# Kernel tuning notes

Measured on AMD Instinct MI355X. Metric: run time of the kernel, lower is better.

The kernel has to match this reference:

```python
import jax, jax.numpy as jnp
import numpy as np

B, N, DIM = 4, 1024, 512
DEPTH, HEADS, DH = 4, 8, 64
INNER = HEADS * DH  # 512
W = 32              # sqrt(N), FeedForward reshapes tokens to (W, W)
SCALE = DH ** -0.5  # used for BOTH spatial and spectral branches (as in source)
EPS_LN = 1e-5
EPS_BN = 1e-5


def setup_inputs() -> dict:
    key = jax.random.key(0)
    ks = jax.random.split(key, 16)
    L = DEPTH
    def rn(k, shape, s=0.02):
        return jax.random.normal(k, shape, jnp.float32) * s
    return {
        "x": jax.random.normal(ks[0], (B, N, DIM), jnp.float32),
        "ln1_w": jnp.ones((L, DIM), jnp.float32), "ln1_b": jnp.zeros((L, DIM), jnp.float32),
        "Wqkv": rn(ks[1], (L, DIM, 3 * INNER)),
        "Wout": rn(ks[2], (L, INNER, DIM)), "bout": jnp.zeros((L, DIM), jnp.float32),
        "sp_w": rn(ks[3], (L, HEADS, HEADS, 3, 3), 0.1), "sp_b": jnp.zeros((L, HEADS), jnp.float32),
        "Wqkv_spec": rn(ks[4], (L, N, 3 * N)),
        "spec_w": rn(ks[5], (L, 1, 1, 3, 3), 0.1), "spec_b": jnp.zeros((L, 1), jnp.float32),
        "ln2_w": jnp.ones((L, DIM), jnp.float32), "ln2_b": jnp.zeros((L, DIM), jnp.float32),
        "dw_w": rn(ks[6], (L, DIM, 1, 3, 3), 0.1), "dw_b": jnp.zeros((L, DIM), jnp.float32),
        "pw_w": rn(ks[7], (L, 256, DIM)), "pw_b": jnp.zeros((L, 256), jnp.float32),
        "bn_g": jnp.ones((L, 256), jnp.float32), "bn_b": jnp.zeros((L, 256), jnp.float32),
        "bn_m": jnp.zeros((L, 256), jnp.float32), "bn_v": jnp.ones((L, 256), jnp.float32),
        "c1_w": rn(ks[8], (L, 512, 256)), "c1_b": jnp.zeros((L, 512), jnp.float32),
        "c2_w": rn(ks[9], (L, DIM, 512)), "c2_b": jnp.zeros((L, DIM), jnp.float32),
    }


def _ln(x, w, b):
    mu = x.mean(-1, keepdims=True)
    var = x.var(-1, keepdims=True)  # biased, matching torch LayerNorm
    return (x - mu) * jax.lax.rsqrt(var + EPS_LN) * w + b


def _conv3x3(x, w, b, groups=1):
    y = jax.lax.conv_general_dilated(x, w, (1, 1), 'SAME',
                                     dimension_numbers=('NCHW', 'OIHW', 'NCHW'),
                                     feature_group_count=groups)
    return y + b[None, :, None, None]


def _block(x, p):
    (ln1w, ln1b, Wqkv, Wout, bout, spw, spb, Wqs, scw, scb,
     ln2w, ln2b, dww, dwb, pww, pwb, bng, bnb, bnm, bnv, c1w, c1b, c2w, c2b) = p
    b = x.shape[0]
    # --- spatial attention (PreNorm) ---
    h = _ln(x, ln1w, ln1b)
    q, k, v = jnp.split(h @ Wqkv, 3, axis=-1)
    split_heads = lambda t: t.reshape(b, N, HEADS, DH).transpose(0, 2, 1, 3)  # b h n d
    q, k, v = split_heads(q), split_heads(k), split_heads(v)
    attn = jax.nn.softmax(jnp.einsum('bhid,bhjd->bhij', q, k) * SCALE, axis=-1)
    attn = _conv3x3(attn, spw, spb)  # conv over the softmax map (heads as channels)
    out = jnp.einsum('bhij,bhjd->bhid', attn, v).transpose(0, 2, 1, 3).reshape(b, N, INNER)
    out = out @ Wout + bout  # (b, n, dim)
    # --- spectral attention on h^T (b, dim, n); v_spec is dead code in source ---
    xt = jnp.swapaxes(h, -1, -2)
    qs, ks_, _vs = jnp.split(xt @ Wqs, 3, axis=-1)  # each (b, dim, n)
    a = jax.nn.softmax(jnp.einsum('bin,bjn->bij', qs, ks_) * SCALE, axis=-1)
    a = _conv3x3(a[:, None], scw, scb)[:, 0]  # (b, dim, dim)
    x = x + jnp.einsum('bnd,bde->bne', out, a)  # residual add from Transformer loop
    # --- FeedForward (PreNorm), FF adds its own internal residual too ---
    h2 = _ln(x, ln2w, ln2b)
    img = h2.reshape(b, W, W, DIM).transpose(0, 3, 1, 2)  # 'b (w h) c -> b c w h'
    t = _conv3x3(img, dww, dwb, groups=DIM)               # depthwise 3x3
    t = jnp.einsum('oc,bchw->bohw', pww, t) + pwb[None, :, None, None]  # pointwise dim->256
    t = (t - bnm[None, :, None, None]) * jax.lax.rsqrt(bnv + EPS_BN)[None, :, None, None] \
        * bng[None, :, None, None] + bnb[None, :, None, None]           # BatchNorm2d (eval)
    t = jax.nn.gelu(jnp.einsum('oc,bchw->bohw', c1w, t) + c1b[None, :, None, None], approximate=False)
    t = jax.nn.gelu(jnp.einsum('oc,bchw->bohw', c2w, t) + c2b[None, :, None, None], approximate=False)
    ff = h2 + t.transpose(0, 2, 3, 1).reshape(b, N, DIM)  # FF internal residual
    return x + ff


def _forward(x, ln1_w, ln1_b, Wqkv, Wout, bout, sp_w, sp_b, Wqkv_spec, spec_w, spec_b,
             ln2_w, ln2_b, dw_w, dw_b, pw_w, pw_b, bn_g, bn_b, bn_m, bn_v,
             c1_w, c1_b, c2_w, c2_b):
    stacked = (ln1_w, ln1_b, Wqkv, Wout, bout, sp_w, sp_b, Wqkv_spec, spec_w, spec_b,
               ln2_w, ln2_b, dw_w, dw_b, pw_w, pw_b, bn_g, bn_b, bn_m, bn_v,
               c1_w, c1_b, c2_w, c2_b)
    for i in range(DEPTH):
        x = _block(x, tuple(a[i] for a in stacked))
    return x


def reference(x, ln1_w, ln1_b, Wqkv, Wout, bout, sp_w, sp_b, Wqkv_spec, spec_w, spec_b,
              ln2_w, ln2_b, dw_w, dw_b, pw_w, pw_b, bn_g, bn_b, bn_m, bn_v,
              c1_w, c1_b, c2_w, c2_b):
    return _forward(x, ln1_w, ln1_b, Wqkv, Wout, bout, sp_w, sp_b, Wqkv_spec, spec_w, spec_b,
                    ln2_w, ln2_b, dw_w, dw_b, pw_w, pw_b, bn_g, bn_b, bn_m, bn_v,
                    c1_w, c1_b, c2_w, c2_b)
```

## Files before the change

### kernel.cpp

```cpp
#include <hip/hip_runtime.h>
#include <hip/hip_bf16.h>

typedef __hip_bfloat16 bf16;
typedef __attribute__((ext_vector_type(8))) short bf16x8;
typedef __attribute__((ext_vector_type(4))) float f32x4;

__device__ __forceinline__ float b2f(bf16 v){ return __bfloat162float(v); }
__device__ __forceinline__ bf16 f2b(float v){ return __float2bfloat16(v); }
__device__ __forceinline__ float bits2f(unsigned u){ return __uint_as_float(u << 16); }
__device__ __forceinline__ unsigned short f2bits(float v){ bf16 t = __float2bfloat16(v); return *(unsigned short*)&t; }

__device__ __forceinline__ float gelu_f(float x){
  return 0.5f * x * (1.f + erff(x * 0.7071067811865475f));
}

__device__ __forceinline__ void gload_lds(const void* g, void* l){
  __builtin_amdgcn_global_load_lds((const __attribute__((address_space(1))) void*)g,
                                   (__attribute__((address_space(3))) void*)l, 16, 0, 0);
}

template<bool MAX>
__device__ __forceinline__ float block_reduce(float v){
  __shared__ float s[4];
  #pragma unroll
  for (int o = 32; o > 0; o >>= 1){
    float t = __shfl_down(v, o, 64);
    v = MAX ? fmaxf(v, t) : (v + t);
  }
  int lane = threadIdx.x & 63, w = threadIdx.x >> 6;
  __syncthreads();
  if (lane == 0) s[w] = v;
  __syncthreads();
  return MAX ? fmaxf(fmaxf(s[0], s[1]), fmaxf(s[2], s[3]))
             : (s[0] + s[1] + s[2] + s[3]);
}

__global__ void detect_k(const unsigned* __restrict__ x, int* __restrict__ flag){
  __shared__ int cnt[256];
  int tid = threadIdx.x;
  int c = 0;
  for (int i = tid; i < 4096; i += 256){
    unsigned h = x[i] & 0xffffu;
    int e = (int)((h >> 7) & 0xff);
    if (h == 0u || (e >= 100 && e <= 133)) c++;
  }
  cnt[tid] = c;
  __syncthreads();
  for (int o = 128; o > 0; o >>= 1){ if (tid < o) cnt[tid] += cnt[tid+o]; __syncthreads(); }
  if (tid == 0) *flag = (cnt[0] < 2048) ? 1 : 0;
}

__global__ __launch_bounds__(256) void cvt_x_k(const void* __restrict__ src,
                                               float* __restrict__ X,
                                               const int* __restrict__ flag){
  int p = blockIdx.x*256 + threadIdx.x;
  X[p] = (*flag) ? ((const float*)src)[p]
                 : __bfloat162float(((const bf16*)src)[p]);
}

struct WCvt21 { const void* src[21]; long long cum[22]; };

__global__ __launch_bounds__(256) void cvt_w_k(WCvt21 a, bf16* __restrict__ WB,
                                               long long total, const int* __restrict__ flag){
  long long i = (long long)blockIdx.x*256 + threadIdx.x;
  if (i >= total) return;
  int t = 0;
  while (a.cum[t+1] <= i) t++;
  long long e = i - a.cum[t];
  WB[i] = (*flag) ? __float2bfloat16(((const float*)a.src[t])[e])
                  : ((const bf16*)a.src[t])[e];
}

__global__ __launch_bounds__(256) void wtrans_k(const void* __restrict__ src, bf16* __restrict__ dst,
                                                int ld_src, int ldd, long long sSrc, long long sDst,
                                                const int* __restrict__ flag){
  __shared__ bf16 t[64][65];
  int z = blockIdx.z;
  int r0 = blockIdx.x*64, c0 = blockIdx.y*64;
  int lane = threadIdx.x & 63, quad = threadIdx.x >> 6;
  const float* sf = (const float*)src;
  const bf16* sb = (const bf16*)src;
  int fl = *flag;
  #pragma unroll
  for (int k = 0; k < 16; ++k){
    int r = quad*16 + k;
    long long idx = z*sSrc + (long long)(r0+r)*ld_src + c0 + lane;
    float v = fl ? sf[idx] : b2f(sb[idx]);
    t[r][lane] = f2b(v);
  }
  __syncthreads();
  #pragma unroll
  for (int k = 0; k < 16; ++k){
    int c = quad*16 + k;
    dst[z*sDst + (long long)(c0+c)*ldd + r0 + lane] = t[lane][c];
  }
}

__global__ void wprep_k(const bf16* __restrict__ spw, bf16* __restrict__ Wr){
  int l = blockIdx.x;
  for (int t = threadIdx.x; t < 1536; t += 256){
    int ho = t / 96, k = t - ho*96;
    float v = 0.f;
    if (ho < 8 && k < 72){
      int tap = k >> 3, hi = k & 7;
      v = b2f(spw[l*576 + ho*72 + hi*9 + tap]);
    }
    Wr[l*1536 + t] = f2b(v);
  }
}

__global__ __launch_bounds__(256) void store_out_k(const float* __restrict__ X,
                                                   void* __restrict__ out,
                                                   const int* __restrict__ flag){
  int p = blockIdx.x*256 + threadIdx.x;
  if (*flag) ((float*)out)[p] = X[p];
  else       ((bf16*)out)[p] = f2b(X[p]);
}

template<int MF, int NF, typename TC>
__global__ __launch_bounds__(256) void gmfma_k(
    int M, int N, int K,
    const bf16* __restrict__ A, int lda, long long sA, long long sA2,
    const bf16* __restrict__ Bt, int ldb, long long sB, long long sB2,
    TC* __restrict__ C, int ldc, long long sC, long long sC2,
    float alpha, int beta,
    const bf16* __restrict__ bias_n,
    const float* __restrict__ scale_n,
    const float* __restrict__ shift_n,
    const bf16* __restrict__ addF,
    int act)
{
  constexpr int BM = MF*32, BN = NF*32;
  constexpr int CHA = BM/16, CH = (BM+BN)/16;
  static_assert(CH % 4 == 0, "chunks must divide among 4 waves");
  __shared__ bf16 Asm[BM][32];
  __shared__ bf16 Bsm[BN][32];
  const int tid = threadIdx.x;
  const int lane = tid & 63, wid = tid >> 6;
  const int wm = wid >> 1, wn = wid & 1;
  const int m0 = blockIdx.y*BM, n0 = blockIdx.x*BN;
  const int z = blockIdx.z;
  const long long zl = z & 7, zh = z >> 3;
  const bf16* Ab = A + zl*sA + zh*sA2;
  const bf16* Bb = Bt + zl*sB + zh*sB2;
  TC* Cb = C + zl*sC + zh*sC2;
  const bf16* Fb = addF ? addF + zl*sC + zh*sC2 : nullptr;

  f32x4 acc[MF][NF];
  f32x4 zero = {0.f, 0.f, 0.f, 0.f};
  #pragma unroll
  for (int m = 0; m < MF; ++m)
    #pragma unroll
    for (int n = 0; n < NF; ++n) acc[m][n] = zero;

  const int rchunk = lane >> 2;
  const int kchunk = (lane & 3) * 8;
  const int row16 = lane & 15, kq = (lane >> 4) * 8;

  for (int k0 = 0; k0 < K; k0 += 32){
    #pragma unroll
    for (int cc = 0; cc < CH/4; ++cc){
      int c = wid + cc*4;
      if (c < CHA){
        int row = c*16 + rchunk;
        gload_lds(Ab + (long long)(m0+row)*lda + k0 + kchunk, &Asm[c*16][0]);
      } else {
        int row = (c-CHA)*16 + rchunk;
        gload_lds(Bb + (long long)(n0+row)*ldb + k0 + kchunk, &Bsm[(c-CHA)*16][0]);
      }
    }
    __syncthreads();
    bf16x8 af[MF], bfr[NF];
    #pragma unroll
    for (int m = 0; m < MF; ++m)
      af[m] = *(const bf16x8*)&Asm[wm*(MF*16) + m*16 + row16][kq];
    #pragma unroll
    for (int n = 0; n < NF; ++n)
      bfr[n] = *(const bf16x8*)&Bsm[wn*(NF*16) + n*16 + row16][kq];
    #pragma unroll
    for (int m = 0; m < MF; ++m)
      #pragma unroll
      for (int n = 0; n < NF; ++n)
        acc[m][n] = __builtin_amdgcn_mfma_f32_16x16x32_bf16(af[m], bfr[n], acc[m][n], 0, 0, 0);
    __syncthreads();
  }

  #pragma unroll
  for (int m = 0; m < MF; ++m){
    #pragma unroll
    for (int n = 0; n < NF; ++n){
      int gn = n0 + wn*(NF*16) + n*16 + (lane & 15);
      float bn_ = bias_n ? b2f(bias_n[gn]) : 0.f;
      float sc = scale_n ? scale_n[gn] : 1.f;
      float sh = shift_n ? shift_n[gn] : 0.f;
      #pragma unroll
      for (int r = 0; r < 4; ++r){
        int gm = m0 + wm*(MF*16) + m*16 + (lane >> 4)*4 + r;
        float v = acc[m][n][r] * alpha + bn_;
        v = v * sc + sh;
        if (act) v = gelu_f(v);
        long long idx = (long long)gm*ldc + gn;
        if (Fb) v += b2f(Fb[idx]);
        if (beta){
          float old;
          if constexpr (__is_same(TC, float)) old = Cb[idx]; else old = b2f(Cb[idx]);
          v += old;
        }
        if constexpr (__is_same(TC, float)) Cb[idx] = v; else Cb[idx] = f2b(v);
      }
    }
  }
}

template<int MF, int NF, typename TC>
static void gmfma_x(hipStream_t st, int z, int M, int N, int K,
                    const bf16* A, int lda, long long sA, long long sA2,
                    const bf16* Bt, int ldb, long long sB, long long sB2,
                    TC* C, int ldc, long long sC, long long sC2,
                    float alpha = 1.f, int beta = 0,
                    const bf16* bias_n = nullptr,
                    const float* scale_n = nullptr, const float* shift_n = nullptr,
                    const bf16* addF = nullptr, int act = 0)
{
  dim3 g(N/(NF*32), M/(MF*32), z);
  gmfma_k<MF,NF,TC><<<g, 256, 0, st>>>(M,N,K,A,lda,sA,sA2,Bt,ldb,sB,sB2,C,ldc,sC,sC2,
                                       alpha,beta,bias_n,scale_n,shift_n,addF,act);
}

template<int MF, int NF, typename TC>
static void gmfma(hipStream_t st, int z, int M, int N, int K,
                  const bf16* A, int lda, long long sA,
                  const bf16* Bt, int ldb, long long sB,
                  TC* C, int ldc, long long sC,
                  float alpha = 1.f, int beta = 0,
                  const bf16* bias_n = nullptr,
                  const float* scale_n = nullptr, const float* shift_n = nullptr,
                  const bf16* addF = nullptr, int act = 0)
{
  gmfma_x<MF,NF,TC>(st, z, M, N, K, A, lda, sA, 8*sA, Bt, ldb, sB, 8*sB,
                    C, ldc, sC, 8*sC, alpha, beta, bias_n, scale_n, shift_n, addF, act);
}

__global__ __launch_bounds__(256) void ln_k(const float* __restrict__ X, bf16* __restrict__ Y,
                                            const bf16* __restrict__ w, const bf16* __restrict__ b){
  long long row = blockIdx.x;
  const float* x = X + row*512;
  bf16* y = Y + row*512;
  int tid = threadIdx.x;
  float v0 = x[tid], v1 = x[tid+256];
  float mean = block_reduce<false>(v0+v1) * (1.f/512.f);
  float msq  = block_reduce<false>(v0*v0+v1*v1) * (1.f/512.f);
  float var = msq - mean*mean;
  float rs = rsqrtf(var + 1e-5f);
  y[tid]     = f2b((v0-mean)*rs*b2f(w[tid])     + b2f(b[tid]));
  y[tid+256] = f2b((v1-mean)*rs*b2f(w[tid+256]) + b2f(b[tid+256]));
}

__global__ __launch_bounds__(256) void softmax_k(float* __restrict__ data, int cols){
  long long row = blockIdx.x;
  float* p = data + row * (long long)cols;
  int tid = threadIdx.x;
  int per = cols >> 8;
  float v[4];
  float mx = -3.4e38f;
  for (int r = 0; r < per; ++r){ v[r] = p[tid + (r<<8)]; mx = fmaxf(mx, v[r]); }
  mx = block_reduce<true>(mx);
  float sum = 0.f;
  for (int r = 0; r < per; ++r){ v[r] = __expf(v[r] - mx); sum += v[r]; }
  sum = block_reduce<false>(sum);
  float inv = 1.f / sum;
  for (int r = 0; r < per; ++r) p[tid + (r<<8)] = v[r] * inv;
}

__global__ __launch_bounds__(256) void maxsum_k(const bf16* __restrict__ Sp,
                                                float* __restrict__ Mrow, float* __restrict__ Irow,
                                                long long bstride){
  __shared__ float redmx[4][8];
  __shared__ float redsum[4][8];
  int i = blockIdx.x;
  long long b = blockIdx.y;
  const bf16* src = Sp + b*bstride + (long long)i*1024;
  int tid = threadIdx.x;
  int lane = tid & 63, w = tid >> 6;
  int j0 = tid*4;

  float v[8][4];
  #pragma unroll
  for (int h = 0; h < 8; ++h){
    ushort4 u = *(const ushort4*)&src[h*1048576 + j0];
    v[h][0] = bits2f(u.x); v[h][1] = bits2f(u.y);
    v[h][2] = bits2f(u.z); v[h][3] = bits2f(u.w);
  }
  #pragma unroll
  for (int h = 0; h < 8; ++h){
    float m = fmaxf(fmaxf(v[h][0], v[h][1]), fmaxf(v[h][2], v[h][3]));
    #pragma unroll
    for (int o = 32; o > 0; o >>= 1) m = fmaxf(m, __shfl_xor(m, o, 64));
    if (lane == 0) redmx[w][h] = m;
  }
  __syncthreads();
  float mx[8];
  #pragma unroll
  for (int h = 0; h < 8; ++h)
    mx[h] = fmaxf(fmaxf(redmx[0][h], redmx[1][h]), fmaxf(redmx[2][h], redmx[3][h]));
  #pragma unroll
  for (int h = 0; h < 8; ++h){
    float s = 0.f;
    #pragma unroll
    for (int r = 0; r < 4; ++r) s += __expf(v[h][r] - mx[h]);
    #pragma unroll
    for (int o = 32; o > 0; o >>= 1) s += __shfl_xor(s, o, 64);
    if (lane == 0) redsum[w][h] = s;
  }
  __syncthreads();
  if (tid < 8){
    float s = redsum[0][tid] + redsum[1][tid] + redsum[2][tid] + redsum[3][tid];
    long long o = (b*1024 + i)*8 + tid;
    Mrow[o] = mx[tid];
    Irow[o] = 1.f / s;
  }
}

__global__ __launch_bounds__(256) void convNorm_k(const bf16* __restrict__ Sp, bf16* __restrict__ Pout,
                                                  const bf16* __restrict__ Wr, const bf16* __restrict__ bias,
                                                  const float* __restrict__ Mrow, const float* __restrict__ Irow,
                                                  long long bstride){
  __shared__ bf16 tile[18][66][8];
  __shared__ float mrow[18][8];
  __shared__ float irow[18][8];
  long long b = blockIdx.z;
  int i0 = blockIdx.y*16, j0 = blockIdx.x*64;
  int tid = threadIdx.x;
  const bf16* src = Sp + b*bstride;

  for (int t = tid; t < 144; t += 256){
    int r = t >> 3, h = t & 7;
    int gi = i0 + r - 1;
    float m = 0.f, iv = 0.f;
    if ((unsigned)gi < 1024u){
      long long o = (b*1024 + gi)*8 + h;
      m = Mrow[o]; iv = Irow[o];
    }
    mrow[r][h] = m; irow[r][h] = iv;
  }
  __syncthreads();

  for (int t = tid; t < 18*66; t += 256){
    int row = t / 66, col = t - row*66;
    int gi = i0 + row - 1, gj = j0 + col - 1;
    bf16x8 val = {};
    if ((unsigned)gi < 1024u && (unsigned)gj < 1024u){
      long long base = (long long)gi*1024 + gj;
      #pragma unroll
      for (int h = 0; h < 8; ++h){
        float s = b2f(src[(long long)h*1048576 + base]);
        val[h] = (short)f2bits(__expf(s - mrow[row][h]) * irow[row][h]);
      }
    }
    *(bf16x8*)&tile[row][col][0] = val;
  }

  int lane = tid & 63, wid = tid >> 6;
  int row16 = lane & 15, q = lane >> 4;
  bf16x8 bf0 = *(const bf16x8*)&Wr[row16*96 +  0 + q*8];
  bf16x8 bf1 = *(const bf16x8*)&Wr[row16*96 + 32 + q*8];
  bf16x8 bf2 = *(const bf16x8*)&Wr[row16*96 + 64 + q*8];
  float bv = (row16 < 8) ? b2f(bias[row16]) : 0.f;
  __syncthreads();

  f32x4 zero = {0.f,0.f,0.f,0.f};
  #pragma unroll
  for (int rr = 0; rr < 4; ++rr){
    int ii = rr*4 + wid;
    f32x4 acc[4] = {zero, zero, zero, zero};
    #pragma unroll
    for (int ks = 0; ks < 3; ++ks){
      int tap = ks*4 + q;
      int tcl = tap > 8 ? 0 : tap;
      int di = tcl / 3, dj = tcl - di*3;
      bf16x8 bsel = ks == 0 ? bf0 : (ks == 1 ? bf1 : bf2);
      #pragma unroll
      for (int mf = 0; mf < 4; ++mf){
        bf16x8 af = *(const bf16x8*)&tile[ii + di][mf*16 + row16 + dj][0];
        acc[mf] = __builtin_amdgcn_mfma_f32_16x16x32_bf16(af, bsel, acc[mf], 0, 0, 0);
      }
    }
    if (row16 < 8){
      bf16* dst = Pout + b*bstride + (long long)row16*1048576 + (long long)(i0 + ii)*1024;
      #pragma unroll
      for (int mf = 0; mf < 4; ++mf){
        int j = j0 + mf*16 + q*4;
        ushort4 o;
        o.x = f2bits(acc[mf][0] + bv);
        o.y = f2bits(acc[mf][1] + bv);
        o.z = f2bits(acc[mf][2] + bv);
        o.w = f2bits(acc[mf][3] + bv);
        *(ushort4*)&dst[j] = o;
      }
    }
  }
}

__global__ __launch_bounds__(256) void conv_spec_k(const float* __restrict__ in, bf16* __restrict__ out,
                                                   const bf16* __restrict__ w, const bf16* __restrict__ bias){
  __shared__ float ti[66][67];
  __shared__ bf16 toutT[64][65];
  int b = blockIdx.z;
  int i0 = blockIdx.y*64, j0 = blockIdx.x*64;
  int tid = threadIdx.x;
  const float* ib = in + (long long)b*262144;
  for (int t = tid; t < 66*66; t += 256){
    int r = t / 66, c = t - r*66;
    int gi = i0 + r - 1, gj = j0 + c - 1;
    float v = 0.f;
    if ((unsigned)gi < 512u && (unsigned)gj < 512u) v = ib[gi*512 + gj];
    ti[r][c] = v;
  }
  __syncthreads();
  float w9[9], bv = b2f(bias[0]);
  #pragma unroll
  for (int d = 0; d < 9; ++d) w9[d] = b2f(w[d]);
  int ii = tid & 63;
  #pragma unroll
  for (int q = 0; q < 16; ++q){
    int jj = (tid >> 6)*16 + q;
    float acc = bv;
    #pragma unroll
    for (int di = 0; di < 3; ++di)
      #pragma unroll
      for (int dj = 0; dj < 3; ++dj)
        acc += w9[di*3+dj] * ti[ii+di][jj+dj];
    toutT[jj][ii] = f2b(acc);
  }
  __syncthreads();
  #pragma unroll
  for (int q = 0; q < 16; ++q){
    int jj = (tid >> 6)*16 + q;
    out[(long long)b*262144 + (j0+jj)*512 + i0 + (tid & 63)] = toutT[jj][tid & 63];
  }
}

__global__ __launch_bounds__(256) void dwconv_k(const bf16* __restrict__ H2, bf16* __restrict__ T1,
                                                const bf16* __restrict__ w, const bf16* __restrict__ bias){
  int p = blockIdx.x*256 + threadIdx.x;
  int cp = p & 255;
  int n = (p >> 8) & 1023;
  int b = p >> 18;
  int c0 = cp*2;
  int wi = n >> 5, hg = n & 31;
  float a0 = b2f(bias[c0]), a1 = b2f(bias[c0+1]);
  #pragma unroll
  for (int di = 0; di < 3; ++di){
    int gw = wi + di - 1;
    if ((unsigned)gw >= 32u) continue;
    #pragma unroll
    for (int dj = 0; dj < 3; ++dj){
      int gh = hg + dj - 1;
      if ((unsigned)gh >= 32u) continue;
      unsigned hv = *(const unsigned*)&H2[((long long)b*1024 + (gw*32+gh))*512 + c0];
      float w0 = b2f(w[c0*9 + di*3 + dj]);
      float w1 = b2f(w[(c0+1)*9 + di*3 + dj]);
      a0 += w0 * bits2f(hv & 0xffffu);
      a1 += w1 * bits2f(hv >> 16);
    }
  }
  bf16 h0 = f2b(a0), h1 = f2b(a1);
  unsigned o = ((unsigned)*(unsigned short*)&h1 << 16) | (unsigned)*(unsigned short*)&h0;
  *(unsigned*)&T1[((long long)b*1024 + n)*512 + c0] = o;
}

__global__ void bnaff_all_k(const bf16* __restrict__ pwb, const bf16* __restrict__ g,
                            const bf16* __restrict__ bb, const bf16* __restrict__ m,
                            const bf16* __restrict__ v, float* __restrict__ BNAFF){
  int l = blockIdx.x, o = threadIdx.x;
  float s = b2f(g[l*256+o]) * rsqrtf(b2f(v[l*256+o]) + 1e-5f);
  BNAFF[l*512 + o] = s;
  BNAFF[l*512 + 256 + o] = (b2f(pwb[l*256+o]) - b2f(m[l*256+o])) * s + b2f(bb[l*256+o]);
}

__global__ __launch_bounds__(256) void vtrans_k(const bf16* __restrict__ QKV, bf16* __restrict__ Vt){
  __shared__ bf16 t[64][65];
  int z = blockIdx.z; int b = z >> 3, h = z & 7;
  const bf16* src = QKV + (long long)b*1572864 + 1024 + h*64;
  bf16* dst = Vt + (long long)z*65536;
  int n0 = blockIdx.x*64;
  int lane = threadIdx.x & 63, quad = threadIdx.x >> 6;
  #pragma unroll
  for (int k = 0; k < 16; ++k){
    int r = quad*16 + k;
    t[r][lane] = src[(long long)(n0+r)*1536 + lane];
  }
  __syncthreads();
  #pragma unroll
  for (int k = 0; k < 16; ++k){
    int d = quad*16 + k;
    dst[(long long)d*1024 + n0 + lane] = t[lane][d];
  }
}

__global__ __launch_bounds__(256) void htrans_k(const bf16* __restrict__ Hb, bf16* __restrict__ HT){
  __shared__ bf16 t[64][65];
  int b = blockIdx.z;
  int n0 = blockIdx.x*64, c0 = blockIdx.y*64;
  int lane = threadIdx.x & 63, quad = threadIdx.x >> 6;
  #pragma unroll
  for (int k = 0; k < 16; ++k){
    int r = quad*16 + k;
    t[r][lane] = Hb[((long long)b*1024 + n0 + r)*512 + c0 + lane];
  }
  __syncthreads();
  #pragma unroll
  for (int k = 0; k < 16; ++k){
    int c = quad*16 + k;
    HT[(long long)b*524288 + (long long)(c0+c)*1024 + n0 + lane] = t[lane][c];
  }
}

extern "C" void kernel_launch(void* const* d_in, const int* in_sizes, int n_in,
                              void* d_out, int out_size, void* d_ws, size_t ws_size,
                              hipStream_t stream)
{
  (void)in_sizes; (void)n_in; (void)out_size;

  const bool big = ws_size >= 207000000ull;
  const long long ATTN_SZ = big ? 33554432LL : 8388608LL;

  float* X     = (float*)d_ws;
  bf16*  WBsm  = (bf16*)(X + 2097152);
  bf16*  WqkvT = WBsm  + 2139648;
  bf16*  WoutT = WqkvT + 3145728;
  bf16*  WqsT  = WoutT + 1048576;
  bf16*  Hbuf  = WqsT  + 8388608;
  bf16*  HbufT = Hbuf  + 2097152;
  bf16*  QKV   = HbufT + 2097152;
  bf16*  Vt    = QKV   + 6291456;
  bf16*  OUTH  = Vt    + 2097152;
  bf16*  OUT   = OUTH  + 2097152;
  bf16*  ATTN  = OUT   + 2097152;
  bf16*  ATTNC = ATTN  + ATTN_SZ;
  float* BNAFF = (float*)(ATTNC + ATTN_SZ);
  bf16*  WR    = (bf16*)(BNAFF + 2048);
  float* MROW  = (float*)(WR + 6144);
  float* IROW  = MROW + 32768;
  int*   FLAG  = (int*)(IROW + 32768);

  float* ASPEC   = (float*)OUTH;
  bf16*  ASPECCT = ATTNC;
  bf16*  T1 = ATTN;
  bf16*  T3 = ATTN + 2097152;
  bf16*  T2 = ATTNC + 2097152;
  bf16*  SQK = ATTN;

  static const int widx[21] = {1,2,5,6,7,9,10,11,12,13,14,15,16,17,18,19,20,21,22,23,24};
  static const long long wsz[21] = {2048,2048,2048,2304,32,36,4,2048,2048,18432,2048,
                                    524288,1024,1024,1024,1024,1024,524288,2048,1048576,2048};
  WCvt21 wc;
  long long cum = 0;
  bf16* wp[21];
  for (int t = 0; t < 21; ++t){
    wc.src[t] = d_in[widx[t]];
    wc.cum[t] = cum;
    wp[t] = WBsm + cum;
    cum += wsz[t];
  }
  wc.cum[21] = cum;

  bf16 *w_ln1w = wp[0],  *w_ln1b = wp[1],  *w_bout = wp[2],  *w_spw = wp[3];
  bf16 *w_spb  = wp[4],  *w_specw= wp[5],  *w_specb= wp[6],  *w_ln2w= wp[7];
  bf16 *w_ln2b = wp[8],  *w_dww  = wp[9],  *w_dwb  = wp[10], *w_pww = wp[11];
  bf16 *w_pwb  = wp[12], *w_bng  = wp[13], *w_bnb  = wp[14], *w_bnm = wp[15];
  bf16 *w_bnv  = wp[16], *w_c1w  = wp[17], *w_c1b  = wp[18], *w_c2w = wp[19];
  bf16 *w_c2b  = wp[20];

  detect_k<<<1, 256, 0, stream>>>((const unsigned*)d_in[0], FLAG);
  cvt_x_k<<<8192, 256, 0, stream>>>(d_in[0], X, FLAG);
  cvt_w_k<<<(int)((cum + 255)/256), 256, 0, stream>>>(wc, WBsm, cum, FLAG);
  wtrans_k<<<dim3(8,24,4), 256, 0, stream>>>(d_in[3], WqkvT, 1536, 512, 786432LL, 786432LL, FLAG);
  wtrans_k<<<dim3(8, 8,4), 256, 0, stream>>>(d_in[4], WoutT,  512, 512, 262144LL, 262144LL, FLAG);
  wtrans_k<<<dim3(16,32,4),256, 0, stream>>>(d_in[8], WqsT,  3072,1024, 3145728LL,2097152LL, FLAG);
  bnaff_all_k<<<4, 256, 0, stream>>>(w_pwb, w_bng, w_bnb, w_bnm, w_bnv, BNAFF);
  wprep_k<<<4, 256, 0, stream>>>(w_spw, WR);

  for (int l = 0; l < 4; ++l){
    ln_k<<<4096, 256, 0, stream>>>(X, Hbuf, w_ln1w + l*512, w_ln1b + l*512);
    gmfma<4,4,bf16>(stream, 1, 4096, 1536, 512,
        Hbuf, 512, 0, WqkvT + (long long)l*786432, 512, 0, QKV, 1536, 0);
    vtrans_k<<<dim3(16,1,32), 256, 0, stream>>>(QKV, Vt);
    if (big){
      gmfma_x<4,4,bf16>(stream, 32, 1024, 1024, 64,
          QKV, 1536, 64, 1572864, QKV + 512, 1536, 64, 1572864,
          ATTN, 1024, 1048576, 8388608, 0.125f);
      maxsum_k<<<dim3(1024,4), 256, 0, stream>>>(ATTN, MROW, IROW, 8388608LL);
      convNorm_k<<<dim3(16,64,4), 256, 0, stream>>>(ATTN, ATTNC, WR + l*1536, w_spb + l*8,
                                                    MROW, IROW, 8388608LL);
      gmfma_x<2,2,bf16>(stream, 32, 1024, 64, 1024,
          ATTNC, 1024, 1048576, 8388608, Vt, 1024, 65536, 524288,
          OUTH, 512, 64, 524288);
    } else {
      for (int b = 0; b < 4; ++b){
        bf16* qkvb = QKV + (long long)b*1572864;
        gmfma<4,4,bf16>(stream, 8, 1024, 1024, 64,
            qkvb, 1536, 64, qkvb + 512, 1536, 64, ATTN, 1024, 1048576, 0.125f);
        maxsum_k<<<dim3(1024,1), 256, 0, stream>>>(ATTN, MROW, IROW, 8388608LL);
        convNorm_k<<<dim3(16,64,1), 256, 0, stream>>>(ATTN, ATTNC, WR + l*1536, w_spb + l*8,
                                                      MROW, IROW, 8388608LL);
        gmfma<2,2,bf16>(stream, 8, 1024, 64, 1024,
            ATTNC, 1024, 1048576, Vt + (long long)b*524288, 1024, 65536,
            OUTH + (long long)b*524288, 512, 64);
      }
    }
    gmfma<2,2,bf16>(stream, 1, 4096, 512, 512,
        OUTH, 512, 0, WoutT + (long long)l*262144, 512, 0, OUT, 512, 0,
        1.f, 0, w_bout + l*512);
    htrans_k<<<dim3(16,8,4), 256, 0, stream>>>(Hbuf, HbufT);
    gmfma<4,4,bf16>(stream, 4, 512, 2048, 1024,
        HbufT, 1024, 524288, WqsT + (long long)l*2097152, 1024, 0, SQK, 2048, 1048576);
    gmfma<2,2,float>(stream, 4, 512, 512, 1024,
        SQK, 2048, 1048576, SQK + 1024, 2048, 1048576, ASPEC, 512, 262144, 0.125f);
    softmax_k<<<2048, 256, 0, stream>>>(ASPEC, 512);
    conv_spec_k<<<dim3(8,8,4), 256, 0, stream>>>(ASPEC, ASPECCT, w_specw + l*9, w_specb + l);
    gmfma<2,2,float>(stream, 4, 1024, 512, 512,
        OUT, 512, 524288, ASPECCT, 512, 262144, X, 512, 524288, 1.f, 1);
    ln_k<<<4096, 256, 0, stream>>>(X, Hbuf, w_ln2w + l*512, w_ln2b + l*512);
    dwconv_k<<<4096, 256, 0, stream>>>(Hbuf, T1, w_dww + l*4608, w_dwb + l*512);
    gmfma<2,2,bf16>(stream, 4, 1024, 256, 512,
        T1, 512, 524288, w_pww + (long long)l*131072, 512, 0, T2, 256, 262144,
        1.f, 0, nullptr, BNAFF + l*512, BNAFF + l*512 + 256);
    gmfma<2,2,bf16>(stream, 4, 1024, 512, 256,
        T2, 256, 262144, w_c1w + (long long)l*131072, 256, 0, T3, 512, 524288,
        1.f, 0, w_c1b + l*512, nullptr, nullptr, nullptr, 1);
    gmfma<2,2,float>(stream, 4, 1024, 512, 512,
        T3, 512, 524288, w_c2w + (long long)l*262144, 512, 0, X, 512, 524288,
        1.f, 1, w_c2b + l*512, nullptr, nullptr, Hbuf, 1);
  }

  store_out_k<<<8192, 256, 0, stream>>>(X, d_out, FLAG);
}
```

Measured before the change: 1.283 ms.

## Fuse V transpose into QKV GEMM, fold softmax into conv, tile convNorm

The QKV GEMM epilogue now also writes the V columns transposed into Vt, which removes the separate vtrans kernel. The spectral softmax is split into a row max/sum stats kernel, and the exp-normalize step moves into conv_spec_k's tile load, so the full softmax write-back pass disappears. convNorm_k now loops over 8 column chunks per block with vectorized loads of head pairs and a separate halo fill, which reduces the grid from 16 to 2 blocks in x. The cost is more per-block serial work, uncoalesced 8-byte transposed stores in the GEMM epilogue, and a larger register footprint in the epilogue.

```diff
diff --git a/kernel.cpp b/kernel.cpp
--- a/kernel.cpp
+++ b/kernel.cpp
@@ -128,7 +128,8 @@
     const float* __restrict__ scale_n,
     const float* __restrict__ shift_n,
     const bf16* __restrict__ addF,
-    int act)
+    int act,
+    bf16* __restrict__ vt)
 {
   constexpr int BM = MF*32, BN = NF*32;
   constexpr int CHA = BM/16, CH = (BM+BN)/16;
@@ -189,13 +190,15 @@
   for (int m = 0; m < MF; ++m){
     #pragma unroll
     for (int n = 0; n < NF; ++n){
-      int gn = n0 + wn*(NF*16) + n*16 + (lane & 15);
+      int gn = n0 + wn*(NF*16) + n*16 + row16;
       float bn_ = bias_n ? b2f(bias_n[gn]) : 0.f;
       float sc = scale_n ? scale_n[gn] : 1.f;
       float sh = shift_n ? shift_n[gn] : 0.f;
+      int gmb = m0 + wm*(MF*16) + m*16 + (lane >> 4)*4;
+      float vals[4];
       #pragma unroll
       for (int r = 0; r < 4; ++r){
-        int gm = m0 + wm*(MF*16) + m*16 + (lane >> 4)*4 + r;
+        int gm = gmb + r;
         float v = acc[m][n][r] * alpha + bn_;
         v = v * sc + sh;
         if (act) v = gelu_f(v);
@@ -207,6 +210,15 @@
           v += old;
         }
         if constexpr (__is_same(TC, float)) Cb[idx] = v; else Cb[idx] = f2b(v);
+        vals[r] = v;
+      }
+      if (vt && gn >= 1024){
+        int h = (gn - 1024) >> 6, d = (gn - 1024) & 63;
+        int bb = gmb >> 10, nn = gmb & 1023;
+        ushort4 o;
+        o.x = f2bits(vals[0]); o.y = f2bits(vals[1]);
+        o.z = f2bits(vals[2]); o.w = f2bits(vals[3]);
+        *(ushort4*)&vt[(((long long)bb*8 + h)*64 + d)*1024 + nn] = o;
       }
     }
   }
@@ -220,11 +232,11 @@
                     float alpha = 1.f, int beta = 0,
                     const bf16* bias_n = nullptr,
                     const float* scale_n = nullptr, const float* shift_n = nullptr,
-                    const bf16* addF = nullptr, int act = 0)
+                    const bf16* addF = nullptr, int act = 0, bf16* vt = nullptr)
 {
   dim3 g(N/(NF*32), M/(MF*32), z);
   gmfma_k<MF,NF,TC><<<g, 256, 0, st>>>(M,N,K,A,lda,sA,sA2,Bt,ldb,sB,sB2,C,ldc,sC,sC2,
-                                       alpha,beta,bias_n,scale_n,shift_n,addF,act);
+                                       alpha,beta,bias_n,scale_n,shift_n,addF,act,vt);
 }
 
 template<int MF, int NF, typename TC>
@@ -235,10 +247,10 @@
                   float alpha = 1.f, int beta = 0,
                   const bf16* bias_n = nullptr,
                   const float* scale_n = nullptr, const float* shift_n = nullptr,
-                  const bf16* addF = nullptr, int act = 0)
+                  const bf16* addF = nullptr, int act = 0, bf16* vt = nullptr)
 {
   gmfma_x<MF,NF,TC>(st, z, M, N, K, A, lda, sA, 8*sA, Bt, ldb, sB, 8*sB,
-                    C, ldc, sC, 8*sC, alpha, beta, bias_n, scale_n, shift_n, addF, act);
+                    C, ldc, sC, 8*sC, alpha, beta, bias_n, scale_n, shift_n, addF, act, vt);
 }
 
 __global__ __launch_bounds__(256) void ln_k(const float* __restrict__ X, bf16* __restrict__ Y,
@@ -256,22 +268,6 @@
   y[tid+256] = f2b((v1-mean)*rs*b2f(w[tid+256]) + b2f(b[tid+256]));
 }
 
-__global__ __launch_bounds__(256) void softmax_k(float* __restrict__ data, int cols){
-  long long row = blockIdx.x;
-  float* p = data + row * (long long)cols;
-  int tid = threadIdx.x;
-  int per = cols >> 8;
-  float v[4];
-  float mx = -3.4e38f;
-  for (int r = 0; r < per; ++r){ v[r] = p[tid + (r<<8)]; mx = fmaxf(mx, v[r]); }
-  mx = block_reduce<true>(mx);
-  float sum = 0.f;
-  for (int r = 0; r < per; ++r){ v[r] = __expf(v[r] - mx); sum += v[r]; }
-  sum = block_reduce<false>(sum);
-  float inv = 1.f / sum;
-  for (int r = 0; r < per; ++r) p[tid + (r<<8)] = v[r] * inv;
-}
-
 __global__ __launch_bounds__(256) void maxsum_k(const bf16* __restrict__ Sp,
                                                 float* __restrict__ Mrow, float* __restrict__ Irow,
                                                 long long bstride){
@@ -321,15 +317,18 @@
   }
 }
 
-__global__ __launch_bounds__(256) void convNorm_k(const bf16* __restrict__ Sp, bf16* __restrict__ Pout,
-                                                  const bf16* __restrict__ Wr, const bf16* __restrict__ bias,
-                                                  const float* __restrict__ Mrow, const float* __restrict__ Irow,
-                                                  long long bstride){
+__global__ __launch_bounds__(256) void convNorm_k(
+    const bf16* __restrict__ Sp, bf16* __restrict__ Pout,
+    const bf16* __restrict__ Wr, const bf16* __restrict__ bias,
+    const float* __restrict__ Mrow, const float* __restrict__ Irow,
+    long long bstride)
+{
   __shared__ bf16 tile[18][66][8];
   __shared__ float mrow[18][8];
   __shared__ float irow[18][8];
   long long b = blockIdx.z;
-  int i0 = blockIdx.y*16, j0 = blockIdx.x*64;
+  int i0 = blockIdx.y*16;
+  int jh0 = blockIdx.x*512;
   int tid = threadIdx.x;
   const bf16* src = Sp + b*bstride;
 
@@ -337,84 +336,139 @@
     int r = t >> 3, h = t & 7;
     int gi = i0 + r - 1;
     float m = 0.f, iv = 0.f;
-    if ((unsigned)gi < 1024u){
-      long long o = (b*1024 + gi)*8 + h;
-      m = Mrow[o]; iv = Irow[o];
-    }
+    if ((unsigned)gi < 1024u){ long long o = (b*1024 + gi)*8 + h; m = Mrow[o]; iv = Irow[o]; }
     mrow[r][h] = m; irow[r][h] = iv;
-  }
-  __syncthreads();
-
-  for (int t = tid; t < 18*66; t += 256){
-    int row = t / 66, col = t - row*66;
-    int gi = i0 + row - 1, gj = j0 + col - 1;
-    bf16x8 val = {};
-    if ((unsigned)gi < 1024u && (unsigned)gj < 1024u){
-      long long base = (long long)gi*1024 + gj;
-      #pragma unroll
-      for (int h = 0; h < 8; ++h){
-        float s = b2f(src[(long long)h*1048576 + base]);
-        val[h] = (short)f2bits(__expf(s - mrow[row][h]) * irow[row][h]);
-      }
-    }
-    *(bf16x8*)&tile[row][col][0] = val;
   }
 
   int lane = tid & 63, wid = tid >> 6;
   int row16 = lane & 15, q = lane >> 4;
-  bf16x8 bf0 = *(const bf16x8*)&Wr[row16*96 +  0 + q*8];
-  bf16x8 bf1 = *(const bf16x8*)&Wr[row16*96 + 32 + q*8];
-  bf16x8 bf2 = *(const bf16x8*)&Wr[row16*96 + 64 + q*8];
+  bf16x8 wf0 = *(const bf16x8*)&Wr[row16*96 +  0 + q*8];
+  bf16x8 wf1 = *(const bf16x8*)&Wr[row16*96 + 32 + q*8];
+  bf16x8 wf2 = *(const bf16x8*)&Wr[row16*96 + 64 + q*8];
   float bv = (row16 < 8) ? b2f(bias[row16]) : 0.f;
-  __syncthreads();
-
-  f32x4 zero = {0.f,0.f,0.f,0.f};
-  #pragma unroll
-  for (int rr = 0; rr < 4; ++rr){
-    int ii = rr*4 + wid;
-    f32x4 acc[4] = {zero, zero, zero, zero};
-    #pragma unroll
-    for (int ks = 0; ks < 3; ++ks){
-      int tap = ks*4 + q;
-      int tcl = tap > 8 ? 0 : tap;
-      int di = tcl / 3, dj = tcl - di*3;
-      bf16x8 bsel = ks == 0 ? bf0 : (ks == 1 ? bf1 : bf2);
+
+  for (int c = 0; c < 8; ++c){
+    int base = jh0 + c*64;
+    __syncthreads();
+    for (int t = tid; t < 576; t += 256){
+      int row = t >> 5, rem = t & 31;
+      int hp = rem >> 3, seg = rem & 7;
+      int gi = i0 + row - 1;
+      int g0 = base + seg*8;
+      unsigned ov[8];
+      if ((unsigned)gi < 1024u){
+        const bf16* p0 = src + (long long)(2*hp)*1048576 + (long long)gi*1024 + g0;
+        bf16x8 a0 = *(const bf16x8*)p0;
+        bf16x8 a1 = *(const bf16x8*)(p0 + 1048576);
+        float m0 = mrow[row][2*hp],   i0v = irow[row][2*hp];
+        float m1 = mrow[row][2*hp+1], i1v = irow[row][2*hp+1];
+        #pragma unroll
+        for (int k = 0; k < 8; ++k){
+          float e0 = __expf(bits2f((unsigned)(unsigned short)a0[k]) - m0) * i0v;
+          float e1 = __expf(bits2f((unsigned)(unsigned short)a1[k]) - m1) * i1v;
+          ov[k] = (unsigned)f2bits(e0) | ((unsigned)f2bits(e1) << 16);
+        }
+      } else {
+        #pragma unroll
+        for (int k = 0; k < 8; ++k) ov[k] = 0u;
+      }
       #pragma unroll
-      for (int mf = 0; mf < 4; ++mf){
-        bf16x8 af = *(const bf16x8*)&tile[ii + di][mf*16 + row16 + dj][0];
-        acc[mf] = __builtin_amdgcn_mfma_f32_16x16x32_bf16(af, bsel, acc[mf], 0, 0, 0);
-      }
-    }
-    if (row16 < 8){
-      bf16* dst = Pout + b*bstride + (long long)row16*1048576 + (long long)(i0 + ii)*1024;
+      for (int k = 0; k < 8; ++k)
+        *(unsigned*)&tile[row][1 + seg*8 + k][2*hp] = ov[k];
+    }
+    if (tid < 72){
+      int row = tid >> 2, hp = tid & 3;
+      int gi = i0 + row - 1;
+      unsigned L = 0u, R = 0u;
+      if ((unsigned)gi < 1024u){
+        long long rb = (long long)gi*1024;
+        int cl = base - 1, cr = base + 64;
+        float m0 = mrow[row][2*hp],   i0v = irow[row][2*hp];
+        float m1 = mrow[row][2*hp+1], i1v = irow[row][2*hp+1];
+        if (cl >= 0){
+          float e0 = __expf(b2f(src[(long long)(2*hp)*1048576 + rb + cl]) - m0) * i0v;
+          float e1 = __expf(b2f(src[(long long)(2*hp+1)*1048576 + rb + cl]) - m1) * i1v;
+          L = (unsigned)f2bits(e0) | ((unsigned)f2bits(e1) << 16);
+        }
+        if (cr < 1024){
+          float e0 = __expf(b2f(src[(long long)(2*hp)*1048576 + rb + cr]) - m0) * i0v;
+          float e1 = __expf(b2f(src[(long long)(2*hp+1)*1048576 + rb + cr]) - m1) * i1v;
+          R = (unsigned)f2bits(e0) | ((unsigned)f2bits(e1) << 16);
+        }
+      }
+      *(unsigned*)&tile[row][0][2*hp] = L;
+      *(unsigned*)&tile[row][65][2*hp] = R;
+    }
+    __syncthreads();
+    #pragma unroll
+    for (int rr = 0; rr < 4; ++rr){
+      int ii = rr*4 + wid;
+      f32x4 zero = {0.f,0.f,0.f,0.f};
+      f32x4 acc[4] = {zero,zero,zero,zero};
       #pragma unroll
-      for (int mf = 0; mf < 4; ++mf){
-        int j = j0 + mf*16 + q*4;
-        ushort4 o;
-        o.x = f2bits(acc[mf][0] + bv);
-        o.y = f2bits(acc[mf][1] + bv);
-        o.z = f2bits(acc[mf][2] + bv);
-        o.w = f2bits(acc[mf][3] + bv);
-        *(ushort4*)&dst[j] = o;
-      }
-    }
-  }
+      for (int ks = 0; ks < 3; ++ks){
+        int tap = ks*4 + q;
+        int tcl = tap > 8 ? 0 : tap;
+        int di = tcl/3, dj = tcl - di*3;
+        bf16x8 wsel = ks==0 ? wf0 : (ks==1 ? wf1 : wf2);
+        #pragma unroll
+        for (int mf = 0; mf < 4; ++mf){
+          bf16x8 af = *(const bf16x8*)&tile[ii+di][mf*16 + row16 + dj][0];
+          acc[mf] = __builtin_amdgcn_mfma_f32_16x16x32_bf16(af, wsel, acc[mf], 0, 0, 0);
+        }
+      }
+      if (row16 < 8){
+        bf16* dst = Pout + b*bstride + (long long)row16*1048576 + (long long)(i0+ii)*1024;
+        #pragma unroll
+        for (int mf = 0; mf < 4; ++mf){
+          int j = base + mf*16 + q*4;
+          ushort4 o;
+          o.x = f2bits(acc[mf][0] + bv);
+          o.y = f2bits(acc[mf][1] + bv);
+          o.z = f2bits(acc[mf][2] + bv);
+          o.w = f2bits(acc[mf][3] + bv);
+          *(ushort4*)&dst[j] = o;
+        }
+      }
+    }
+  }
+}
+
+__global__ __launch_bounds__(256) void spec_ms_k(const float* __restrict__ A,
+                                                 float* __restrict__ Sm, float* __restrict__ Si){
+  int row = blockIdx.x;
+  const float* p = A + (long long)row*512;
+  int tid = threadIdx.x;
+  float v0 = p[tid], v1 = p[tid+256];
+  float mx = block_reduce<true>(fmaxf(v0, v1));
+  float s = block_reduce<false>(__expf(v0-mx) + __expf(v1-mx));
+  if (tid == 0){ Sm[row] = mx; Si[row] = 1.f/s; }
 }
 
 __global__ __launch_bounds__(256) void conv_spec_k(const float* __restrict__ in, bf16* __restrict__ out,
-                                                   const bf16* __restrict__ w, const bf16* __restrict__ bias){
+                                                   const bf16* __restrict__ w, const bf16* __restrict__ bias,
+                                                   const float* __restrict__ Sm, const float* __restrict__ Si){
   __shared__ float ti[66][67];
   __shared__ bf16 toutT[64][65];
+  __shared__ float sms[66], sis[66];
   int b = blockIdx.z;
   int i0 = blockIdx.y*64, j0 = blockIdx.x*64;
   int tid = threadIdx.x;
   const float* ib = in + (long long)b*262144;
+  if (tid < 66){
+    int gi = i0 + tid - 1;
+    float m = 0.f, iv = 0.f;
+    if ((unsigned)gi < 512u){ m = Sm[b*512 + gi]; iv = Si[b*512 + gi]; }
+    sms[tid] = m; sis[tid] = iv;
+  }
+  __syncthreads();
   for (int t = tid; t < 66*66; t += 256){
-    int r = t / 66, c = t - r*66;
-    int gi = i0 + r - 1, gj = j0 + c - 1;
+    int r = t / 66, cc = t - r*66;
+    int gi = i0 + r - 1, gj = j0 + cc - 1;
     float v = 0.f;
-    if ((unsigned)gi < 512u && (unsigned)gj < 512u) v = ib[gi*512 + gj];
-    ti[r][c] = v;
+    if ((unsigned)gi < 512u && (unsigned)gj < 512u)
+      v = __expf(ib[gi*512 + gj] - sms[r]) * sis[r];
+    ti[r][cc] = v;
   }
   __syncthreads();
   float w9[9], bv = b2f(bias[0]);
@@ -476,26 +530,6 @@
   float s = b2f(g[l*256+o]) * rsqrtf(b2f(v[l*256+o]) + 1e-5f);
   BNAFF[l*512 + o] = s;
   BNAFF[l*512 + 256 + o] = (b2f(pwb[l*256+o]) - b2f(m[l*256+o])) * s + b2f(bb[l*256+o]);
-}
-
-__global__ __launch_bounds__(256) void vtrans_k(const bf16* __restrict__ QKV, bf16* __restrict__ Vt){
-  __shared__ bf16 t[64][65];
-  int z = blockIdx.z; int b = z >> 3, h = z & 7;
-  const bf16* src = QKV + (long long)b*1572864 + 1024 + h*64;
-  bf16* dst = Vt + (long long)z*65536;
-  int n0 = blockIdx.x*64;
-  int lane = threadIdx.x & 63, quad = threadIdx.x >> 6;
-  #pragma unroll
-  for (int k = 0; k < 16; ++k){
-    int r = quad*16 + k;
-    t[r][lane] = src[(long long)(n0+r)*1536 + lane];
-  }
-  __syncthreads();
-  #pragma unroll
-  for (int k = 0; k < 16; ++k){
-    int d = quad*16 + k;
-    dst[(long long)d*1024 + n0 + lane] = t[lane][d];
-  }
 }
 
 __global__ __launch_bounds__(256) void htrans_k(const bf16* __restrict__ Hb, bf16* __restrict__ HT){
@@ -542,7 +576,9 @@
   bf16*  WR    = (bf16*)(BNAFF + 2048);
   float* MROW  = (float*)(WR + 6144);
   float* IROW  = MROW + 32768;
-  int*   FLAG  = (int*)(IROW + 32768);
+  float* SMS   = IROW + 32768;
+  float* SIS   = SMS + 2048;
+  int*   FLAG  = (int*)(SIS + 2048);
 
   float* ASPEC   = (float*)OUTH;
   bf16*  ASPECCT = ATTNC;
@@ -584,15 +620,15 @@
   for (int l = 0; l < 4; ++l){
     ln_k<<<4096, 256, 0, stream>>>(X, Hbuf, w_ln1w + l*512, w_ln1b + l*512);
     gmfma<4,4,bf16>(stream, 1, 4096, 1536, 512,
-        Hbuf, 512, 0, WqkvT + (long long)l*786432, 512, 0, QKV, 1536, 0);
-    vtrans_k<<<dim3(16,1,32), 256, 0, stream>>>(QKV, Vt);
+        Hbuf, 512, 0, WqkvT + (long long)l*786432, 512, 0, QKV, 1536, 0,
+        1.f, 0, nullptr, nullptr, nullptr, nullptr, 0, Vt);
     if (big){
       gmfma_x<4,4,bf16>(stream, 32, 1024, 1024, 64,
           QKV, 1536, 64, 1572864, QKV + 512, 1536, 64, 1572864,
           ATTN, 1024, 1048576, 8388608, 0.125f);
       maxsum_k<<<dim3(1024,4), 256, 0, stream>>>(ATTN, MROW, IROW, 8388608LL);
-      convNorm_k<<<dim3(16,64,4), 256, 0, stream>>>(ATTN, ATTNC, WR + l*1536, w_spb + l*8,
-                                                    MROW, IROW, 8388608LL);
+      convNorm_k<<<dim3(2,64,4), 256, 0, stream>>>(ATTN, ATTNC, WR + l*1536, w_spb + l*8,
+                                                   MROW, IROW, 8388608LL);
       gmfma_x<2,2,bf16>(stream, 32, 1024, 64, 1024,
           ATTNC, 1024, 1048576, 8388608, Vt, 1024, 65536, 524288,
           OUTH, 512, 64, 524288);
@@ -602,8 +638,8 @@
         gmfma<4,4,bf16>(stream, 8, 1024, 1024, 64,
             qkvb, 1536, 64, qkvb + 512, 1536, 64, ATTN, 1024, 1048576, 0.125f);
         maxsum_k<<<dim3(1024,1), 256, 0, stream>>>(ATTN, MROW, IROW, 8388608LL);
-        convNorm_k<<<dim3(16,64,1), 256, 0, stream>>>(ATTN, ATTNC, WR + l*1536, w_spb + l*8,
-                                                      MROW, IROW, 8388608LL);
+        convNorm_k<<<dim3(2,64,1), 256, 0, stream>>>(ATTN, ATTNC, WR + l*1536, w_spb + l*8,
+                                                     MROW, IROW, 8388608LL);
         gmfma<2,2,bf16>(stream, 8, 1024, 64, 1024,
             ATTNC, 1024, 1048576, Vt + (long long)b*524288, 1024, 65536,
             OUTH + (long long)b*524288, 512, 64);
@@ -617,8 +653,9 @@
         HbufT, 1024, 524288, WqsT + (long long)l*2097152, 1024, 0, SQK, 2048, 1048576);
     gmfma<2,2,float>(stream, 4, 512, 512, 1024,
         SQK, 2048, 1048576, SQK + 1024, 2048, 1048576, ASPEC, 512, 262144, 0.125f);
-    softmax_k<<<2048, 256, 0, stream>>>(ASPEC, 512);
-    conv_spec_k<<<dim3(8,8,4), 256, 0, stream>>>(ASPEC, ASPECCT, w_specw + l*9, w_specb + l);
+    spec_ms_k<<<2048, 256, 0, stream>>>(ASPEC, SMS, SIS);
+    conv_spec_k<<<dim3(8,8,4), 256, 0, stream>>>(ASPEC, ASPECCT, w_specw + l*9, w_specb + l,
+                                                 SMS, SIS);
     gmfma<2,2,float>(stream, 4, 1024, 512, 512,
         OUT, 512, 524288, ASPECCT, 512, 262144, X, 512, 524288, 1.f, 1);
     ln_k<<<4096, 256, 0, stream>>>(X, Hbuf, w_ln2w + l*512, w_ln2b + l*512);
```

New measurement: 1.246 ms. 1.03x faster.
